# Performance work log

Measured on AMD Instinct MI355X. Metric: run time of the kernel, lower is better.

## Reference

```python
import jax, jax.numpy as jnp
import numpy as np

Q = 3
MAX_SHIFT = 4.0


def setup_inputs() -> dict:
    key = jax.random.key(0)
    k1, k2, k3, k4 = jax.random.split(key, 4)
    x = jax.random.normal(k1, (16, 64, 128, 128), jnp.float32)
    weight = jax.random.normal(k2, (64, 192, 3, 3), jnp.float32) * 0.05
    bias = jax.random.normal(k3, (64,), jnp.float32) * 0.05
    # shift_init='random': uniform in [-1, 1]; forward multiplies by max_shift
    shifts = jax.random.uniform(k4, (64, 2), jnp.float32, -1.0, 1.0)
    return {"x": x, "weight": weight, "bias": bias, "shifts": shifts}


def _shift_bilinear(x, shifts, max_shift):
    """Per-channel bilinear translation, matching affine_grid+grid_sample
    (align_corners=False, padding_mode='zeros').
    x: [N,C,H,W]; shifts: [C,2] with (sx, sy) in normalized units.
    Sample location for output (i,j) is (i + sy*max_shift, j + sx*max_shift)."""
    N, C, H, W = x.shape
    sx = shifts[:, 0] * max_shift  # pixels along width
    sy = shifts[:, 1] * max_shift  # pixels along height
    ys = jnp.arange(H, dtype=x.dtype)[None, :] + sy[:, None]  # [C,H]
    xs = jnp.arange(W, dtype=x.dtype)[None, :] + sx[:, None]  # [C,W]
    y0f = jnp.floor(ys); fy = ys - y0f; y0 = y0f.astype(jnp.int32); y1 = y0 + 1
    x0f = jnp.floor(xs); fx = xs - x0f; x0 = x0f.astype(jnp.int32); x1 = x0 + 1

    def gather(yi, xi):
        vy = (yi >= 0) & (yi < H)          # [C,H]
        vx = (xi >= 0) & (xi < W)          # [C,W]
        yc = jnp.clip(yi, 0, H - 1)
        xc = jnp.clip(xi, 0, W - 1)
        g = jnp.take_along_axis(x, yc[None, :, :, None], axis=2)
        g = jnp.take_along_axis(g, xc[None, :, None, :], axis=3)
        m = (vy[:, :, None] & vx[:, None, :]).astype(x.dtype)[None]
        return g * m

    w00 = ((1 - fy)[:, :, None] * (1 - fx)[:, None, :])[None]
    w01 = ((1 - fy)[:, :, None] * fx[:, None, :])[None]
    w10 = (fy[:, :, None] * (1 - fx)[:, None, :])[None]
    w11 = (fy[:, :, None] * fx[:, None, :])[None]
    return (w00 * gather(y0, x0) + w01 * gather(y0, x1)
            + w10 * gather(y1, x0) + w11 * gather(y1, x1))


def reference(x, weight, bias, shifts):
    # 1) per-channel learnless shift (grid_sample bilinear, zeros padding)
    xs = _shift_bilinear(x, shifts, MAX_SHIFT)
    # 2) Maclaurin power series: concat(x, x^2, ..., x^q) on channels -> [N, C*q, H, W]
    xq = jnp.concatenate([xs ** i for i in range(1, Q + 1)], axis=1)
    # 3) dense conv (groups=1), stride 1, padding 1
    out = jax.lax.conv_general_dilated(
        xq, weight, window_strides=(1, 1), padding=((1, 1), (1, 1)),
        dimension_numbers=("NCHW", "OIHW", "NCHW"))
    return out + bias[None, :, None, None]
```

## Files before the change

### kernel.cpp

```cpp
#include <hip/hip_runtime.h>
#include <hip/hip_bf16.h>
#include <math.h>

#define NB 16
#define C_IN 64
#define C_OUT 64
#define HH 128
#define WW 128
#define MAX_SHIFT 4.0f

typedef __attribute__((ext_vector_type(8))) short bf16x8;
typedef __attribute__((ext_vector_type(4))) float f32x4;
typedef __attribute__((ext_vector_type(4))) unsigned int u32x4;

__device__ inline unsigned short bf16_rne(float f) {
    unsigned u = __builtin_bit_cast(unsigned, f);
    u += 0x7fffu + ((u >> 16) & 1u);
    return (unsigned short)(u >> 16);
}
__device__ inline unsigned pack_bf16x2(float lo, float hi) {
    unsigned ul = __builtin_bit_cast(unsigned, lo);
    unsigned uh = __builtin_bit_cast(unsigned, hi);
    ul += 0x7fffu + ((ul >> 16) & 1u);
    uh += 0x7fffu + ((uh >> 16) & 1u);
    return (ul >> 16) | (uh & 0xffff0000u);
}

#define CPAD 66

__global__ __launch_bounds__(256)
void shift_v(const float* __restrict__ x, const float* __restrict__ shifts,
             unsigned short* __restrict__ xv) {
    __shared__ unsigned short row[64 * CPAD];
    __shared__ float s_fx[C_IN], s_fy[C_IN];
    __shared__ int s_dx[C_IN], s_dy[C_IN];

    int b = blockIdx.x;
    int wh = b & 1;
    int h  = (b >> 1) & 127;
    int n  = b >> 8;
    int tid = threadIdx.x;
    int wv = tid >> 6;
    int l  = tid & 63;

    if (tid < C_IN) {
        float sx = shifts[2 * tid] * MAX_SHIFT;
        float sy = shifts[2 * tid + 1] * MAX_SHIFT;
        float fx0 = floorf(sx), fy0 = floorf(sy);
        s_dx[tid] = (int)fx0; s_dy[tid] = (int)fy0;
        s_fx[tid] = sx - fx0;  s_fy[tid] = sy - fy0;
    }
    __syncthreads();

    const float* xn = x + (size_t)n * (C_IN * HH * WW);
    int w = wh * 64 + l;
    unsigned short* rw = row + l * CPAD;

    #pragma unroll 4
    for (int it = 0; it < 16; ++it) {
        int c = it * 4 + wv;
        int dx = s_dx[c], dy = s_dy[c];
        float fx = s_fx[c], fy = s_fy[c];
        const float* xp = xn + (size_t)c * (HH * WW);
        int y0 = h + dy, y1 = y0 + 1;
        bool vy0 = ((unsigned)y0 < (unsigned)HH);
        bool vy1 = ((unsigned)y1 < (unsigned)HH);
        const float* r0 = xp + y0 * WW;
        const float* r1 = xp + y1 * WW;

        int x0 = w + dx, x1 = x0 + 1;
        bool vx0 = ((unsigned)x0 < (unsigned)WW);
        bool vx1 = ((unsigned)x1 < (unsigned)WW);
        float v00 = (vy0 && vx0) ? r0[x0] : 0.f;
        float v01 = (vy0 && vx1) ? r0[x1] : 0.f;
        float v10 = (vy1 && vx0) ? r1[x0] : 0.f;
        float v11 = (vy1 && vx1) ? r1[x1] : 0.f;
        float v = (1.f - fy) * ((1.f - fx) * v00 + fx * v01)
                + fy * ((1.f - fx) * v10 + fx * v11);
        rw[c] = bf16_rne(v);
    }
    __syncthreads();

    const unsigned* rp = (const unsigned*)row;
    unsigned* dst = (unsigned*)xv + ((size_t)((n * HH + h) * WW) + wh * 64) * 32;
    #pragma unroll
    for (int itw = 0; itw < 8; ++itw) {
        int o32 = itw * 256 + tid;
        int wl = o32 >> 5;
        int c4 = o32 & 31;
        dst[o32] = rp[wl * (CPAD / 2) + c4];
    }
}

__global__ void prep_w3(const float* __restrict__ w, unsigned short* __restrict__ wbuf) {
    int id = blockIdx.x * 256 + threadIdx.x;
    int e = id & 7;
    int l = (id >> 3) & 63;
    int f = id >> 9;
    int mf = f & 3;
    int f2 = f >> 2;
    int kb = f2 % 6;
    int t  = f2 / 6;
    int cg = kb / 3;
    int p  = kb - cg * 3;
    int cl = (l >> 4) * 8 + e;
    int co = mf * 16 + (l & 15);
    wbuf[id] = bf16_rne(w[(co * 192 + p * 64 + cg * 32 + cl) * 9 + t]);
}

__global__ __launch_bounds__(256, 2)
void conv2b(const unsigned short* __restrict__ xv,
            const unsigned short* __restrict__ wbuf,
            const float* __restrict__ bias,
            float* __restrict__ out) {
    __shared__ unsigned short tile[324 * 100];

    int bid = blockIdx.x;
    int wg = (bid & 7) * 128 + (bid >> 3);
    int n  = wg >> 6;
    int t6 = wg & 63;
    int i0 = (t6 >> 3) * 16;
    int j0 = (t6 & 7) * 16;

    int tid = threadIdx.x;
    int l  = tid & 63;
    int wv = tid >> 6;
    int lm = l & 15;
    int lg = l >> 4;

    f32x4 acc[4][4];
    #pragma unroll
    for (int mf = 0; mf < 4; ++mf) {
        #pragma unroll
        for (int r = 0; r < 4; ++r) {
            float bv = bias[mf * 16 + lg * 4 + r];
            #pragma unroll
            for (int nf = 0; nf < 4; ++nf) acc[mf][nf][r] = bv;
        }
    }

    const unsigned short* xn = xv + (size_t)n * (HH * WW * 64);

    #pragma unroll 1
    for (int cg = 0; cg < 2; ++cg) {
        __syncthreads();
        #pragma unroll
        for (int it = 0; it < 6; ++it) {
            int item = it * 256 + tid;
            if (item < 1296) {
                int px = item >> 2, chunk = item & 3;
                int rr = px / 18;
                int cc = px - rr * 18;
                int gi = i0 - 1 + rr, gj = j0 - 1 + cc;
                u32x4 dv = {0, 0, 0, 0};
                if ((unsigned)gi < (unsigned)HH && (unsigned)gj < (unsigned)WW)
                    dv = *(const u32x4*)(xn + ((size_t)gi * WW + gj) * 64 + cg * 32 + chunk * 8);
                unsigned o2[4], o3[4];
                #pragma unroll
                for (int q = 0; q < 4; ++q) {
                    unsigned u = dv[q];
                    float f0 = __builtin_bit_cast(float, u << 16);
                    float f1 = __builtin_bit_cast(float, u & 0xffff0000u);
                    float p20 = f0 * f0, p21 = f1 * f1;
                    float p30 = p20 * f0, p31 = p21 * f1;
                    o2[q] = pack_bf16x2(p20, p21);
                    o3[q] = pack_bf16x2(p30, p31);
                }
                char* rec = (char*)tile + px * 200 + chunk * 16;
                *(u32x4*)(rec)       = dv;
                *(u32x4*)(rec + 64)  = (u32x4){o2[0], o2[1], o2[2], o2[3]};
                *(u32x4*)(rec + 128) = (u32x4){o3[0], o3[1], o3[2], o3[3]};
            }
        }
        __syncthreads();

        #pragma unroll 1
        for (int p = 0; p < 3; ++p) {
            int kb = cg * 3 + p;
            bf16x8 Af[4];
            #pragma unroll
            for (int mf = 0; mf < 4; ++mf)
                Af[mf] = *(const bf16x8*)(wbuf + (size_t)((0 * 6 + kb) * 4 + mf) * 512 + l * 8);

            #pragma unroll 1
            for (int t = 0; t < 9; ++t) {
                bf16x8 Afn[4];
                int tn = (t < 8) ? t + 1 : t;
                #pragma unroll
                for (int mf = 0; mf < 4; ++mf)
                    Afn[mf] = *(const bf16x8*)(wbuf + (size_t)((tn * 6 + kb) * 4 + mf) * 512 + l * 8);

                int ky = t / 3, kx = t - ky * 3;
                #pragma unroll
                for (int nf = 0; nf < 4; ++nf) {
                    int off = ((wv * 4 + nf + ky) * 18 + (lm + kx)) * 200 + p * 64 + lg * 16;
                    bf16x8 bfrag = *(const bf16x8*)((const char*)tile + off);
                    #pragma unroll
                    for (int mf = 0; mf < 4; ++mf)
                        acc[mf][nf] = __builtin_amdgcn_mfma_f32_16x16x32_bf16(Af[mf], bfrag, acc[mf][nf], 0, 0, 0);
                }
                #pragma unroll
                for (int mf = 0; mf < 4; ++mf) Af[mf] = Afn[mf];
            }
        }
    }

    #pragma unroll
    for (int mf = 0; mf < 4; ++mf) {
        #pragma unroll
        for (int nf = 0; nf < 4; ++nf) {
            int rowi = i0 + wv * 4 + nf;
            int col = j0 + lm;
            #pragma unroll
            for (int r = 0; r < 4; ++r) {
                int co = mf * 16 + lg * 4 + r;
                out[(((size_t)n * C_OUT + co) * HH + rowi) * WW + col] = acc[mf][nf][r];
            }
        }
    }
}

#define S_PX 100

__global__ __launch_bounds__(256, 2)
void conv_f(const float* __restrict__ x,
            const float* __restrict__ shifts,
            const unsigned short* __restrict__ wbuf,
            const float* __restrict__ bias,
            float* __restrict__ out) {
    __shared__ unsigned short tile[324 * S_PX];
    __shared__ float s_fx[C_IN], s_fy[C_IN];
    __shared__ int s_dx[C_IN], s_dy[C_IN];

    int bid = blockIdx.x;
    int wg = (bid & 7) * 128 + (bid >> 3);
    int n  = wg >> 6;
    int t6 = wg & 63;
    int i0 = (t6 >> 3) * 16;
    int j0 = (t6 & 7) * 16;

    int tid = threadIdx.x;
    int l  = tid & 63;
    int wv = tid >> 6;
    int lm = l & 15;
    int lg = l >> 4;

    if (tid < C_IN) {
        float sx = shifts[2 * tid] * MAX_SHIFT;
        float sy = shifts[2 * tid + 1] * MAX_SHIFT;
        float fx0 = floorf(sx), fy0 = floorf(sy);
        s_dx[tid] = (int)fx0; s_dy[tid] = (int)fy0;
        s_fx[tid] = sx - fx0;  s_fy[tid] = sy - fy0;
    }

    f32x4 acc[4][4];
    #pragma unroll
    for (int mf = 0; mf < 4; ++mf) {
        #pragma unroll
        for (int r = 0; r < 4; ++r) {
            float bv = bias[mf * 16 + lg * 4 + r];
            #pragma unroll
            for (int nf = 0; nf < 4; ++nf) acc[mf][nf][r] = bv;
        }
    }

    const float* xn = x + (size_t)n * (C_IN * HH * WW);

    #pragma unroll 1
    for (int cg = 0; cg < 2; ++cg) {
        __syncthreads();
        #pragma unroll 2
        for (int it = 0; it < 21; ++it) {
            int item = it * 256 + tid;
            if (item < 5184) {
                int cl  = item / 162;
                int rem = item - cl * 162;
                int rp  = rem / 18;
                int cc  = rem - rp * 18;
                int c   = cg * 32 + cl;
                int dx = s_dx[c], dy = s_dy[c];
                float fx = s_fx[c], fy = s_fy[c];
                const float* xp = xn + (size_t)c * (HH * WW);

                int gj  = j0 - 1 + cc;
                int xx0 = gj + dx, xx1 = xx0 + 1;
                bool vx0 = ((unsigned)xx0 < (unsigned)WW);
                bool vx1 = ((unsigned)xx1 < (unsigned)WW);
                int gi0 = i0 - 1 + rp * 2;
                int y0  = gi0 + dy;
                bool vyA = ((unsigned)y0 < (unsigned)HH);
                bool vyB = ((unsigned)(y0 + 1) < (unsigned)HH);
                bool vyC = ((unsigned)(y0 + 2) < (unsigned)HH);
                const float* rA = xp + y0 * WW;
                const float* rB = rA + WW;
                const float* rC = rB + WW;
                float m0 = (vyA && vx0) ? rA[xx0] : 0.f;
                float m1 = (vyA && vx1) ? rA[xx1] : 0.f;
                float m2 = (vyB && vx0) ? rB[xx0] : 0.f;
                float m3 = (vyB && vx1) ? rB[xx1] : 0.f;
                float m4 = (vyC && vx0) ? rC[xx0] : 0.f;
                float m5 = (vyC && vx1) ? rC[xx1] : 0.f;
                float hA = (1.f - fx) * m0 + fx * m1;
                float hB = (1.f - fx) * m2 + fx * m3;
                float hC = (1.f - fx) * m4 + fx * m5;
                float vT = (1.f - fy) * hA + fy * hB;
                float vU = (1.f - fy) * hB + fy * hC;
                if (!((unsigned)gj < (unsigned)WW))        { vT = 0.f; vU = 0.f; }
                if (!((unsigned)gi0 < (unsigned)HH))       vT = 0.f;
                if (!((unsigned)(gi0 + 1) < (unsigned)HH)) vU = 0.f;

                float t2 = vT * vT, t3 = t2 * vT;
                float u2 = vU * vU, u3 = u2 * vU;
                unsigned short* recT = tile + (rp * 2 * 18 + cc) * S_PX;
                unsigned short* recU = recT + 18 * S_PX;
                recT[cl]      = bf16_rne(vT);
                recT[32 + cl] = bf16_rne(t2);
                recT[64 + cl] = bf16_rne(t3);
                recU[cl]      = bf16_rne(vU);
                recU[32 + cl] = bf16_rne(u2);
                recU[64 + cl] = bf16_rne(u3);
            }
        }
        __syncthreads();

        #pragma unroll 1
        for (int p = 0; p < 3; ++p) {
            int kb = cg * 3 + p;
            bf16x8 Af[4];
            #pragma unroll
            for (int mf = 0; mf < 4; ++mf)
                Af[mf] = *(const bf16x8*)(wbuf + (size_t)((0 * 6 + kb) * 4 + mf) * 512 + l * 8);

            #pragma unroll 1
            for (int t = 0; t < 9; ++t) {
                bf16x8 Afn[4];
                int tn = (t < 8) ? t + 1 : t;
                #pragma unroll
                for (int mf = 0; mf < 4; ++mf)
                    Afn[mf] = *(const bf16x8*)(wbuf + (size_t)((tn * 6 + kb) * 4 + mf) * 512 + l * 8);

                int ky = t / 3, kx = t - ky * 3;
                #pragma unroll
                for (int nf = 0; nf < 4; ++nf) {
                    int off = ((wv * 4 + nf + ky) * 18 + (lm + kx)) * 200 + p * 64 + lg * 16;
                    bf16x8 bfrag = *(const bf16x8*)((const char*)tile + off);
                    #pragma unroll
                    for (int mf = 0; mf < 4; ++mf)
                        acc[mf][nf] = __builtin_amdgcn_mfma_f32_16x16x32_bf16(Af[mf], bfrag, acc[mf][nf], 0, 0, 0);
                }
                #pragma unroll
                for (int mf = 0; mf < 4; ++mf) Af[mf] = Afn[mf];
            }
        }
    }

    #pragma unroll
    for (int mf = 0; mf < 4; ++mf) {
        #pragma unroll
        for (int nf = 0; nf < 4; ++nf) {
            int rowi = i0 + wv * 4 + nf;
            int col = j0 + lm;
            #pragma unroll
            for (int r = 0; r < 4; ++r) {
                int co = mf * 16 + lg * 4 + r;
                out[(((size_t)n * C_OUT + co) * HH + rowi) * WW + col] = acc[mf][nf][r];
            }
        }
    }
}

extern "C" void kernel_launch(void* const* d_in, const int* in_sizes, int n_in,
                              void* d_out, int out_size, void* d_ws, size_t ws_size,
                              hipStream_t stream) {
    (void)in_sizes; (void)n_in; (void)out_size;
    const float* x      = (const float*)d_in[0];
    const float* weight = (const float*)d_in[1];
    const float* bias   = (const float*)d_in[2];
    const float* shifts = (const float*)d_in[3];
    float* out = (float*)d_out;

    const size_t xv_elems = (size_t)NB * HH * WW * 64;
    const size_t need2 = xv_elems * 2 + 110592 * 2;

    if (ws_size >= need2) {
        unsigned short* xv   = (unsigned short*)d_ws;
        unsigned short* wbuf = xv + xv_elems;
        prep_w3<<<432, 256, 0, stream>>>(weight, wbuf);
        shift_v<<<NB * HH * 2, 256, 0, stream>>>(x, shifts, xv);
        conv2b<<<1024, 256, 0, stream>>>(xv, wbuf, bias, out);
    } else {
        unsigned short* wbuf = (unsigned short*)d_ws;
        prep_w3<<<432, 256, 0, stream>>>(weight, wbuf);
        conv_f<<<1024, 256, 0, stream>>>(x, shifts, wbuf, bias, out);
    }
}
```

Before: 106.6 us.

## Restage conv input per K-block with smaller LDS tile and reordered weights

Replaces the conv kernel that staged all three power terms for 32 channels at once with one that stages only the 32 channel-power combinations for each K-block, cutting the LDS tile from 200 to 80 bytes per pixel. Weights are re-packed so each K-block mixes two 16-channel groups by power. This reduces shared memory footprint and per-stage conversion work, but adds three times as many stage loads and barriers and rereads the input halo more often.

```diff
diff --git a/kernel.cpp b/kernel.cpp
--- a/kernel.cpp
+++ b/kernel.cpp
@@ -91,6 +91,138 @@
         dst[o32] = rp[wl * (CPAD / 2) + c4];
     }
 }
+
+__global__ void prep_w4(const float* __restrict__ w, unsigned short* __restrict__ wbuf) {
+    int id = blockIdx.x * 256 + threadIdx.x;
+    int e = id & 7;
+    int l = (id >> 3) & 63;
+    int f = id >> 9;
+    int mf = f & 3;
+    int f2 = f >> 2;
+    int kb = f2 % 6;
+    int t  = f2 / 6;
+    int s  = (l >> 4) * 8 + e;
+    int ci = kb * 2 + (s >> 4);
+    int g  = ci / 3;
+    int p  = ci - g * 3;
+    int c  = g * 16 + (s & 15);
+    int co = mf * 16 + (l & 15);
+    wbuf[id] = bf16_rne(w[(co * 192 + p * 64 + c) * 9 + t]);
+}
+
+__global__ __launch_bounds__(256, 2)
+void conv2c(const unsigned short* __restrict__ xv,
+            const unsigned short* __restrict__ wbuf,
+            const float* __restrict__ bias,
+            float* __restrict__ out) {
+    __shared__ unsigned short tile[324 * 40];
+
+    int bid = blockIdx.x;
+    int wg = (bid & 7) * 128 + (bid >> 3);
+    int n  = wg >> 6;
+    int t6 = wg & 63;
+    int i0 = (t6 >> 3) * 16;
+    int j0 = (t6 & 7) * 16;
+
+    int tid = threadIdx.x;
+    int l  = tid & 63;
+    int wv = tid >> 6;
+    int lm = l & 15;
+    int lg = l >> 4;
+
+    f32x4 acc[4][4];
+    #pragma unroll
+    for (int mf = 0; mf < 4; ++mf) {
+        #pragma unroll
+        for (int r = 0; r < 4; ++r) {
+            float bv = bias[mf * 16 + lg * 4 + r];
+            #pragma unroll
+            for (int nf = 0; nf < 4; ++nf) acc[mf][nf][r] = bv;
+        }
+    }
+
+    const unsigned short* xn = xv + (size_t)n * (HH * WW * 64);
+
+    #pragma unroll 1
+    for (int kb = 0; kb < 6; ++kb) {
+        __syncthreads();
+        #pragma unroll
+        for (int it = 0; it < 6; ++it) {
+            int item = it * 256 + tid;
+            if (item < 1296) {
+                int px = item >> 2, sub = item & 3;
+                int half = sub >> 1, q = sub & 1;
+                int ci = kb * 2 + half;
+                int g = ci / 3;
+                int p = ci - g * 3;
+                int rr = px / 18;
+                int cc = px - rr * 18;
+                int gi = i0 - 1 + rr, gj = j0 - 1 + cc;
+                u32x4 dv = {0, 0, 0, 0};
+                if ((unsigned)gi < (unsigned)HH && (unsigned)gj < (unsigned)WW)
+                    dv = *(const u32x4*)(xn + ((size_t)gi * WW + gj) * 64 + g * 16 + q * 8);
+                u32x4 ov;
+                #pragma unroll
+                for (int q4 = 0; q4 < 4; ++q4) {
+                    unsigned u = dv[q4];
+                    if (p == 0) {
+                        ov[q4] = u;
+                    } else {
+                        float f0 = __builtin_bit_cast(float, u << 16);
+                        float f1 = __builtin_bit_cast(float, u & 0xffff0000u);
+                        float r0 = f0 * f0, r1 = f1 * f1;
+                        if (p == 2) { r0 *= f0; r1 *= f1; }
+                        ov[q4] = pack_bf16x2(r0, r1);
+                    }
+                }
+                *(u32x4*)((char*)tile + px * 80 + half * 32 + q * 16) = ov;
+            }
+        }
+        __syncthreads();
+
+        bf16x8 Af[4];
+        #pragma unroll
+        for (int mf = 0; mf < 4; ++mf)
+            Af[mf] = *(const bf16x8*)(wbuf + (size_t)((0 * 6 + kb) * 4 + mf) * 512 + l * 8);
+
+        #pragma unroll 1
+        for (int t = 0; t < 9; ++t) {
+            bf16x8 Afn[4];
+            int tn = (t < 8) ? t + 1 : t;
+            #pragma unroll
+            for (int mf = 0; mf < 4; ++mf)
+                Afn[mf] = *(const bf16x8*)(wbuf + (size_t)((tn * 6 + kb) * 4 + mf) * 512 + l * 8);
+
+            int ky = t / 3, kx = t - ky * 3;
+            #pragma unroll
+            for (int nf = 0; nf < 4; ++nf) {
+                int off = ((wv * 4 + nf + ky) * 18 + (lm + kx)) * 80 + lg * 16;
+                bf16x8 bfrag = *(const bf16x8*)((const char*)tile + off);
+                #pragma unroll
+                for (int mf = 0; mf < 4; ++mf)
+                    acc[mf][nf] = __builtin_amdgcn_mfma_f32_16x16x32_bf16(Af[mf], bfrag, acc[mf][nf], 0, 0, 0);
+            }
+            #pragma unroll
+            for (int mf = 0; mf < 4; ++mf) Af[mf] = Afn[mf];
+        }
+    }
+
+    #pragma unroll
+    for (int mf = 0; mf < 4; ++mf) {
+        #pragma unroll
+        for (int nf = 0; nf < 4; ++nf) {
+            int rowi = i0 + wv * 4 + nf;
+            int col = j0 + lm;
+            #pragma unroll
+            for (int r = 0; r < 4; ++r) {
+                int co = mf * 16 + lg * 4 + r;
+                out[(((size_t)n * C_OUT + co) * HH + rowi) * WW + col] = acc[mf][nf][r];
+            }
+        }
+    }
+}
+
+#define S_PX 100
 
 __global__ void prep_w3(const float* __restrict__ w, unsigned short* __restrict__ wbuf) {
     int id = blockIdx.x * 256 + threadIdx.x;
@@ -107,120 +239,6 @@
     int co = mf * 16 + (l & 15);
     wbuf[id] = bf16_rne(w[(co * 192 + p * 64 + cg * 32 + cl) * 9 + t]);
 }
-
-__global__ __launch_bounds__(256, 2)
-void conv2b(const unsigned short* __restrict__ xv,
-            const unsigned short* __restrict__ wbuf,
-            const float* __restrict__ bias,
-            float* __restrict__ out) {
-    __shared__ unsigned short tile[324 * 100];
-
-    int bid = blockIdx.x;
-    int wg = (bid & 7) * 128 + (bid >> 3);
-    int n  = wg >> 6;
-    int t6 = wg & 63;
-    int i0 = (t6 >> 3) * 16;
-    int j0 = (t6 & 7) * 16;
-
-    int tid = threadIdx.x;
-    int l  = tid & 63;
-    int wv = tid >> 6;
-    int lm = l & 15;
-    int lg = l >> 4;
-
-    f32x4 acc[4][4];
-    #pragma unroll
-    for (int mf = 0; mf < 4; ++mf) {
-        #pragma unroll
-        for (int r = 0; r < 4; ++r) {
-            float bv = bias[mf * 16 + lg * 4 + r];
-            #pragma unroll
-            for (int nf = 0; nf < 4; ++nf) acc[mf][nf][r] = bv;
-        }
-    }
-
-    const unsigned short* xn = xv + (size_t)n * (HH * WW * 64);
-
-    #pragma unroll 1
-    for (int cg = 0; cg < 2; ++cg) {
-        __syncthreads();
-        #pragma unroll
-        for (int it = 0; it < 6; ++it) {
-            int item = it * 256 + tid;
-            if (item < 1296) {
-                int px = item >> 2, chunk = item & 3;
-                int rr = px / 18;
-                int cc = px - rr * 18;
-                int gi = i0 - 1 + rr, gj = j0 - 1 + cc;
-                u32x4 dv = {0, 0, 0, 0};
-                if ((unsigned)gi < (unsigned)HH && (unsigned)gj < (unsigned)WW)
-                    dv = *(const u32x4*)(xn + ((size_t)gi * WW + gj) * 64 + cg * 32 + chunk * 8);
-                unsigned o2[4], o3[4];
-                #pragma unroll
-                for (int q = 0; q < 4; ++q) {
-                    unsigned u = dv[q];
-                    float f0 = __builtin_bit_cast(float, u << 16);
-                    float f1 = __builtin_bit_cast(float, u & 0xffff0000u);
-                    float p20 = f0 * f0, p21 = f1 * f1;
-                    float p30 = p20 * f0, p31 = p21 * f1;
-                    o2[q] = pack_bf16x2(p20, p21);
-                    o3[q] = pack_bf16x2(p30, p31);
-                }
-                char* rec = (char*)tile + px * 200 + chunk * 16;
-                *(u32x4*)(rec)       = dv;
-                *(u32x4*)(rec + 64)  = (u32x4){o2[0], o2[1], o2[2], o2[3]};
-                *(u32x4*)(rec + 128) = (u32x4){o3[0], o3[1], o3[2], o3[3]};
-            }
-        }
-        __syncthreads();
-
-        #pragma unroll 1
-        for (int p = 0; p < 3; ++p) {
-            int kb = cg * 3 + p;
-            bf16x8 Af[4];
-            #pragma unroll
-            for (int mf = 0; mf < 4; ++mf)
-                Af[mf] = *(const bf16x8*)(wbuf + (size_t)((0 * 6 + kb) * 4 + mf) * 512 + l * 8);
-
-            #pragma unroll 1
-            for (int t = 0; t < 9; ++t) {
-                bf16x8 Afn[4];
-                int tn = (t < 8) ? t + 1 : t;
-                #pragma unroll
-                for (int mf = 0; mf < 4; ++mf)
-                    Afn[mf] = *(const bf16x8*)(wbuf + (size_t)((tn * 6 + kb) * 4 + mf) * 512 + l * 8);
-
-                int ky = t / 3, kx = t - ky * 3;
-                #pragma unroll
-                for (int nf = 0; nf < 4; ++nf) {
-                    int off = ((wv * 4 + nf + ky) * 18 + (lm + kx)) * 200 + p * 64 + lg * 16;
-                    bf16x8 bfrag = *(const bf16x8*)((const char*)tile + off);
-                    #pragma unroll
-                    for (int mf = 0; mf < 4; ++mf)
-                        acc[mf][nf] = __builtin_amdgcn_mfma_f32_16x16x32_bf16(Af[mf], bfrag, acc[mf][nf], 0, 0, 0);
-                }
-                #pragma unroll
-                for (int mf = 0; mf < 4; ++mf) Af[mf] = Afn[mf];
-            }
-        }
-    }
-
-    #pragma unroll
-    for (int mf = 0; mf < 4; ++mf) {
-        #pragma unroll
-        for (int nf = 0; nf < 4; ++nf) {
-            int rowi = i0 + wv * 4 + nf;
-            int col = j0 + lm;
-            #pragma unroll
-            for (int r = 0; r < 4; ++r) {
-                int co = mf * 16 + lg * 4 + r;
-                out[(((size_t)n * C_OUT + co) * HH + rowi) * WW + col] = acc[mf][nf][r];
-            }
-        }
-    }
-}
-
-#define S_PX 100
 
 __global__ __launch_bounds__(256, 2)
 void conv_f(const float* __restrict__ x,
@@ -385,9 +403,9 @@
     if (ws_size >= need2) {
         unsigned short* xv   = (unsigned short*)d_ws;
         unsigned short* wbuf = xv + xv_elems;
-        prep_w3<<<432, 256, 0, stream>>>(weight, wbuf);
+        prep_w4<<<432, 256, 0, stream>>>(weight, wbuf);
         shift_v<<<NB * HH * 2, 256, 0, stream>>>(x, shifts, xv);
-        conv2b<<<1024, 256, 0, stream>>>(xv, wbuf, bias, out);
+        conv2c<<<1024, 256, 0, stream>>>(xv, wbuf, bias, out);
     } else {
         unsigned short* wbuf = (unsigned short*)d_ws;
         prep_w3<<<432, 256, 0, stream>>>(weight, wbuf);
```

Result: slower. 116.9 us (+9.7%).

## Stage one power slice per tile fill to shrink LDS and raise occupancy

Applied to the files above, without the earlier changes.

The conv kernel now loops over six K-blocks (channel group × power), and each pass reloads the halo tile from global memory and writes only the single needed power (x, x², or x³) into LDS. The shared tile shrinks from about 64 KB to about 28 KB, so more workgroups can fit per CU. In exchange the halo is read from global/L2 three times as often, there are more barriers, and the 88-byte stride may change bank-conflict behaviour.

```diff
diff --git a/kernel.cpp b/kernel.cpp
--- a/kernel.cpp
+++ b/kernel.cpp
@@ -109,11 +109,11 @@
 }
 
 __global__ __launch_bounds__(256, 2)
-void conv2b(const unsigned short* __restrict__ xv,
+void conv2d(const unsigned short* __restrict__ xv,
             const unsigned short* __restrict__ wbuf,
             const float* __restrict__ bias,
             float* __restrict__ out) {
-    __shared__ unsigned short tile[324 * 100];
+    __shared__ unsigned short tile[324 * 44];
 
     int bid = blockIdx.x;
     int wg = (bid & 7) * 128 + (bid >> 3);
@@ -142,66 +142,64 @@
     const unsigned short* xn = xv + (size_t)n * (HH * WW * 64);
 
     #pragma unroll 1
-    for (int cg = 0; cg < 2; ++cg) {
+    for (int kb = 0; kb < 6; ++kb) {
+        int cg = kb / 3;
+        int p  = kb - cg * 3;
         __syncthreads();
         #pragma unroll
         for (int it = 0; it < 6; ++it) {
             int item = it * 256 + tid;
             if (item < 1296) {
-                int px = item >> 2, chunk = item & 3;
+                int px = item >> 2, sub = item & 3;
                 int rr = px / 18;
                 int cc = px - rr * 18;
                 int gi = i0 - 1 + rr, gj = j0 - 1 + cc;
                 u32x4 dv = {0, 0, 0, 0};
                 if ((unsigned)gi < (unsigned)HH && (unsigned)gj < (unsigned)WW)
-                    dv = *(const u32x4*)(xn + ((size_t)gi * WW + gj) * 64 + cg * 32 + chunk * 8);
-                unsigned o2[4], o3[4];
-                #pragma unroll
-                for (int q = 0; q < 4; ++q) {
-                    unsigned u = dv[q];
-                    float f0 = __builtin_bit_cast(float, u << 16);
-                    float f1 = __builtin_bit_cast(float, u & 0xffff0000u);
-                    float p20 = f0 * f0, p21 = f1 * f1;
-                    float p30 = p20 * f0, p31 = p21 * f1;
-                    o2[q] = pack_bf16x2(p20, p21);
-                    o3[q] = pack_bf16x2(p30, p31);
+                    dv = *(const u32x4*)(xn + ((size_t)gi * WW + gj) * 64 + cg * 32 + sub * 8);
+                u32x4 ov;
+                if (p == 0) {
+                    ov = dv;
+                } else {
+                    #pragma unroll
+                    for (int q = 0; q < 4; ++q) {
+                        unsigned u = dv[q];
+                        float f0 = __builtin_bit_cast(float, u << 16);
+                        float f1 = __builtin_bit_cast(float, u & 0xffff0000u);
+                        float r0 = f0 * f0, r1 = f1 * f1;
+                        if (p == 2) { r0 *= f0; r1 *= f1; }
+                        ov[q] = pack_bf16x2(r0, r1);
+                    }
                 }
-                char* rec = (char*)tile + px * 200 + chunk * 16;
-                *(u32x4*)(rec)       = dv;
-                *(u32x4*)(rec + 64)  = (u32x4){o2[0], o2[1], o2[2], o2[3]};
-                *(u32x4*)(rec + 128) = (u32x4){o3[0], o3[1], o3[2], o3[3]};
+                *(u32x4*)((char*)tile + px * 88 + sub * 16) = ov;
             }
         }
         __syncthreads();
 
+        bf16x8 Af[4];
+        #pragma unroll
+        for (int mf = 0; mf < 4; ++mf)
+            Af[mf] = *(const bf16x8*)(wbuf + (size_t)((0 * 6 + kb) * 4 + mf) * 512 + l * 8);
+
         #pragma unroll 1
-        for (int p = 0; p < 3; ++p) {
-            int kb = cg * 3 + p;
-            bf16x8 Af[4];
+        for (int t = 0; t < 9; ++t) {
+            bf16x8 Afn[4];
+            int tn = (t < 8) ? t + 1 : t;
             #pragma unroll
             for (int mf = 0; mf < 4; ++mf)
-                Af[mf] = *(const bf16x8*)(wbuf + (size_t)((0 * 6 + kb) * 4 + mf) * 512 + l * 8);
-
-            #pragma unroll 1
-            for (int t = 0; t < 9; ++t) {
-                bf16x8 Afn[4];
-                int tn = (t < 8) ? t + 1 : t;
+                Afn[mf] = *(const bf16x8*)(wbuf + (size_t)((tn * 6 + kb) * 4 + mf) * 512 + l * 8);
+
+            int ky = t / 3, kx = t - ky * 3;
+            #pragma unroll
+            for (int nf = 0; nf < 4; ++nf) {
+                int off = ((wv * 4 + nf + ky) * 18 + (lm + kx)) * 88 + lg * 16;
+                bf16x8 bfrag = *(const bf16x8*)((const char*)tile + off);
                 #pragma unroll
                 for (int mf = 0; mf < 4; ++mf)
-                    Afn[mf] = *(const bf16x8*)(wbuf + (size_t)((tn * 6 + kb) * 4 + mf) * 512 + l * 8);
-
-                int ky = t / 3, kx = t - ky * 3;
-                #pragma unroll
-                for (int nf = 0; nf < 4; ++nf) {
-                    int off = ((wv * 4 + nf + ky) * 18 + (lm + kx)) * 200 + p * 64 + lg * 16;
-                    bf16x8 bfrag = *(const bf16x8*)((const char*)tile + off);
-                    #pragma unroll
-                    for (int mf = 0; mf < 4; ++mf)
-                        acc[mf][nf] = __builtin_amdgcn_mfma_f32_16x16x32_bf16(Af[mf], bfrag, acc[mf][nf], 0, 0, 0);
-                }
-                #pragma unroll
-                for (int mf = 0; mf < 4; ++mf) Af[mf] = Afn[mf];
-            }
+                    acc[mf][nf] = __builtin_amdgcn_mfma_f32_16x16x32_bf16(Af[mf], bfrag, acc[mf][nf], 0, 0, 0);
+            }
+            #pragma unroll
+            for (int mf = 0; mf < 4; ++mf) Af[mf] = Afn[mf];
         }
     }
 
@@ -387,7 +385,7 @@
         unsigned short* wbuf = xv + xv_elems;
         prep_w3<<<432, 256, 0, stream>>>(weight, wbuf);
         shift_v<<<NB * HH * 2, 256, 0, stream>>>(x, shifts, xv);
-        conv2b<<<1024, 256, 0, stream>>>(xv, wbuf, bias, out);
+        conv2d<<<1024, 256, 0, stream>>>(xv, wbuf, bias, out);
     } else {
         unsigned short* wbuf = (unsigned short*)d_ws;
         prep_w3<<<432, 256, 0, stream>>>(weight, wbuf);
```

Result: slower. 114.2 us (+7.1%).
